# Kernel tuning notes

Hardware: AMD Instinct MI355X
Metric: run time of the kernel (lower is better)

Reference implementation:

```python
import jax, jax.numpy as jnp
import numpy as np

TOKENS_B, TOKENS_S, N_IN, N_OUT = 8, 2048, 4096, 4096
N8, N4 = 2048, 2048  # channels per format


def setup_inputs() -> dict:
    key = jax.random.key(0)
    k = jax.random.split(key, 7)
    x = jax.random.normal(k[0], (TOKENS_B, TOKENS_S, N_IN), dtype=jnp.float32)
    # int8-format group: values in [-128, 127], per-output-channel scale
    q8 = jax.random.randint(k[1], (N8, N_IN), -128, 128, dtype=jnp.int32)
    s8 = jax.random.uniform(k[2], (N8, 1), dtype=jnp.float32) * 0.01 + 1e-4
    # int4-format group: values in [-8, 7], per-output-channel scale
    q4 = jax.random.randint(k[3], (N4, N_IN), -8, 8, dtype=jnp.int32)
    s4 = jax.random.uniform(k[4], (N4, 1), dtype=jnp.float32) * 0.1 + 1e-4
    # inverse permutation restoring original channel order from [fmt8 | fmt4] concat
    inv_perm = jax.random.permutation(k[5], N_OUT).astype(jnp.int32)
    bias = jax.random.normal(k[6], (N_OUT,), dtype=jnp.float32) * 0.01
    return {"x": x, "q8": q8, "s8": s8, "q4": q4, "s4": s4,
            "inv_perm": inv_perm, "bias": bias}


def reference(x, q8, s8, q4, s4, inv_perm, bias):
    # Per-format dequantize: w = q * scale (per-output-channel scale)
    w8 = q8.astype(jnp.float32) * s8  # [N8, N_IN]
    w4 = q4.astype(jnp.float32) * s4  # [N4, N_IN]
    # Grouped GEMMs, one per format
    y8 = jnp.einsum('bsi,oi->bso', x, w8)  # [B, S, N8]
    y4 = jnp.einsum('bsi,oi->bso', x, w4)  # [B, S, N4]
    # Concat along output channels, then restore original channel order
    y = jnp.concatenate([y8, y4], axis=-1)  # [B, S, N_OUT]
    out = y[..., inv_perm] + bias
    return out
```

## Files before the change

### kernel.cpp

```cpp
#include <hip/hip_runtime.h>


#define M_TOK 16384
#define N_O   4096
#define K_IN  4096
#define N8F   2048
#define NT    (K_IN / 128)

typedef __attribute__((ext_vector_type(4))) int i32x4;

__device__ __forceinline__ void gl_lds16(const void* g, void* l) {
  __builtin_amdgcn_global_load_lds(
      (const __attribute__((address_space(1))) unsigned int*)g,
      (__attribute__((address_space(3))) unsigned int*)l, 16, 0, 0);
}

__device__ __forceinline__ int clampq(float f) {
  int q = (int)rintf(f);
  return q > 127 ? 127 : (q < -127 ? -127 : q);
}

__global__ void prep_kernel(const float* __restrict__ x,
                            const int4* __restrict__ q8, const float* __restrict__ s8,
                            const int4* __restrict__ q4, const float* __restrict__ s4,
                            const int* __restrict__ inv,
                            char* __restrict__ Wq, float* __restrict__ scale,
                            float* __restrict__ sx, char* __restrict__ xq) {
  __shared__ float red[4];
  const int t = threadIdx.x;
  if (blockIdx.x < N_O) {
    const int j = blockIdx.x;
    const int c = inv[j];
    const int4* src; float s;
    if (c < N8F) { src = q8 + (size_t)c * (K_IN / 4);         s = s8[c]; }
    else         { src = q4 + (size_t)(c - N8F) * (K_IN / 4); s = s4[c - N8F]; }
    if (t == 0) scale[j] = s;
    unsigned dw[4];
#pragma unroll
    for (int i = 0; i < 4; ++i) {
      int4 v = src[t * 4 + i];
      dw[i] = (v.x & 255) | ((v.y & 255) << 8) | ((v.z & 255) << 16)
            | ((unsigned)(v.w & 255) << 24);
    }
    *(uint4*)(Wq + (size_t)j * K_IN + t * 16) = make_uint4(dw[0], dw[1], dw[2], dw[3]);
  } else {
    const int T = blockIdx.x - N_O;
    const float4* xr = (const float4*)(x + (size_t)T * K_IN);
    float4 v[4];
    float m = 0.f;
#pragma unroll
    for (int i = 0; i < 4; ++i) {
      v[i] = xr[t * 4 + i];
      m = fmaxf(m, fmaxf(fmaxf(fabsf(v[i].x), fabsf(v[i].y)),
                         fmaxf(fabsf(v[i].z), fabsf(v[i].w))));
    }
#pragma unroll
    for (int o = 32; o; o >>= 1) m = fmaxf(m, __shfl_xor(m, o));
    if ((t & 63) == 0) red[t >> 6] = m;
    __syncthreads();
    m = fmaxf(fmaxf(red[0], red[1]), fmaxf(red[2], red[3]));
    const float rq = m > 0.f ? 127.f / m : 0.f;
    if (t == 0) sx[T] = m * (1.f / 127.f);
    unsigned dw[4];
#pragma unroll
    for (int i = 0; i < 4; ++i) {
      int a0 = clampq(v[i].x * rq), a1 = clampq(v[i].y * rq);
      int a2 = clampq(v[i].z * rq), a3 = clampq(v[i].w * rq);
      dw[i] = (a0 & 255) | ((a1 & 255) << 8) | ((a2 & 255) << 16)
            | ((unsigned)(a3 & 255) << 24);
    }
    *(uint4*)(xq + (size_t)T * K_IN + t * 16) = make_uint4(dw[0], dw[1], dw[2], dw[3]);
  }
}

__global__ __launch_bounds__(512, 2)
void gemm_i8(const char* __restrict__ xq, const char* __restrict__ Wq,
             const float* __restrict__ sx, const float* __restrict__ scale,
             const float* __restrict__ bias, float* __restrict__ out) {
  __shared__ __align__(16) char sm[131072];
  const int t = threadIdx.x;
  const int w = t >> 6, l = t & 63;
  const int wr = w >> 2, wc = w & 3;
  const int bm = blockIdx.x >> 4, bn = blockIdx.x & 15;
  const int row0 = bm * 256, col0 = bn * 256;

  const int srow = l >> 3;
  const int schunk = ((l & 7) ^ srow) * 16;
  const char* aG = xq + (size_t)(row0 + w * 16 + srow) * K_IN + schunk;
  const char* bG = Wq + (size_t)(col0 + w * 16 + srow) * K_IN + schunk;
  char* aL0 = sm + w * 2048;
  char* bL0 = sm + 32768 + w * 2048;

  auto stageA = [&](int buf, int kt, int h) {
    const char* g = aG + (size_t)h * (128 * K_IN) + (size_t)kt * 128;
    char* p = aL0 + buf * 65536 + h * 16384;
    gl_lds16(g, p);
    gl_lds16(g + 8 * K_IN, p + 1024);
  };
  auto stageB = [&](int buf, int kt, int h) {
    const char* g = bG + (size_t)h * (128 * K_IN) + (size_t)kt * 128;
    char* p = bL0 + buf * 65536 + h * 16384;
    gl_lds16(g, p);
    gl_lds16(g + 8 * K_IN, p + 1024);
  };

  const int lrow128 = (l & 15) * 128;
  const int cb0 = (((l >> 4) << 4) ^ ((l & 7) << 4));
  const int aWoff = wr * 16384 + lrow128;
  const int bWoff = 32768 + (wc >> 1) * 16384 + (wc & 1) * 8192 + lrow128;

  i32x4 acc[8][4];
#pragma unroll
  for (int m = 0; m < 8; ++m)
#pragma unroll
    for (int n = 0; n < 4; ++n) acc[m][n] = (i32x4){0, 0, 0, 0};

  stageB(0, 0, 0); stageB(0, 0, 1); stageA(0, 0, 0); stageA(0, 0, 1);
  stageB(1, 1, 0); stageB(1, 1, 1); stageA(1, 1, 0);
  asm volatile("s_waitcnt vmcnt(6)" ::: "memory");
  __builtin_amdgcn_s_barrier();

  i32x4 bfr[4][2], afr[2][2], afr2[2][2];

  for (int kt = 0; kt < NT; ++kt) {
    const int cur = kt & 1;
    const char* smA = sm + cur * 65536 + aWoff;
    const char* smB = sm + cur * 65536 + bWoff;

#pragma unroll
    for (int n = 0; n < 4; ++n) {
      bfr[n][0] = *(const i32x4*)(smB + n * 2048 + cb0);
      bfr[n][1] = *(const i32x4*)(smB + n * 2048 + (cb0 ^ 64));
    }
#pragma unroll
    for (int m = 0; m < 2; ++m) {
      afr[m][0] = *(const i32x4*)(smA + m * 2048 + cb0);
      afr[m][1] = *(const i32x4*)(smA + m * 2048 + (cb0 ^ 64));
    }
    if (kt + 1 < NT) stageA(cur ^ 1, kt + 1, 1);
    __builtin_amdgcn_s_barrier();
    asm volatile("s_waitcnt lgkmcnt(0)" ::: "memory");
    __builtin_amdgcn_s_setprio(1);
#pragma unroll
    for (int m = 0; m < 2; ++m)
#pragma unroll
      for (int n = 0; n < 4; ++n)
#pragma unroll
        for (int kk = 0; kk < 2; ++kk)
          acc[m][n] = __builtin_amdgcn_mfma_i32_16x16x64_i8(afr[m][kk], bfr[n][kk],
                                                            acc[m][n], 0, 0, 0);
    __builtin_amdgcn_s_setprio(0);
    __builtin_amdgcn_s_barrier();

#pragma unroll
    for (int m = 0; m < 2; ++m) {
      afr[m][0] = *(const i32x4*)(smA + (2 + m) * 2048 + cb0);
      afr[m][1] = *(const i32x4*)(smA + (2 + m) * 2048 + (cb0 ^ 64));
    }
    if (kt + 2 < NT) stageB(cur, kt + 2, 0);
    __builtin_amdgcn_s_barrier();
    asm volatile("s_waitcnt lgkmcnt(0)" ::: "memory");
    __builtin_amdgcn_s_setprio(1);
#pragma unroll
    for (int m = 0; m < 2; ++m)
#pragma unroll
      for (int n = 0; n < 4; ++n)
#pragma unroll
        for (int kk = 0; kk < 2; ++kk)
          acc[2 + m][n] = __builtin_amdgcn_mfma_i32_16x16x64_i8(afr[m][kk], bfr[n][kk],
                                                                acc[2 + m][n], 0, 0, 0);
    __builtin_amdgcn_s_setprio(0);
    __builtin_amdgcn_s_barrier();

#pragma unroll
    for (int m = 0; m < 2; ++m) {
      afr[m][0]  = *(const i32x4*)(smA + (4 + m) * 2048 + cb0);
      afr[m][1]  = *(const i32x4*)(smA + (4 + m) * 2048 + (cb0 ^ 64));
      afr2[m][0] = *(const i32x4*)(smA + (6 + m) * 2048 + cb0);
      afr2[m][1] = *(const i32x4*)(smA + (6 + m) * 2048 + (cb0 ^ 64));
    }
    if (kt + 2 < NT) stageB(cur, kt + 2, 1);
    __builtin_amdgcn_s_barrier();
    asm volatile("s_waitcnt lgkmcnt(0)" ::: "memory");
    __builtin_amdgcn_s_setprio(1);
#pragma unroll
    for (int m = 0; m < 2; ++m)
#pragma unroll
      for (int n = 0; n < 4; ++n)
#pragma unroll
        for (int kk = 0; kk < 2; ++kk)
          acc[4 + m][n] = __builtin_amdgcn_mfma_i32_16x16x64_i8(afr[m][kk], bfr[n][kk],
                                                                acc[4 + m][n], 0, 0, 0);
    __builtin_amdgcn_s_setprio(0);
    __builtin_amdgcn_s_barrier();

    if (kt + 2 < NT) {
      stageA(cur, kt + 2, 0);
      asm volatile("s_waitcnt vmcnt(6)" ::: "memory");
    } else {
      asm volatile("s_waitcnt vmcnt(0)" ::: "memory");
    }
    __builtin_amdgcn_s_barrier();
    __builtin_amdgcn_s_setprio(1);
#pragma unroll
    for (int m = 0; m < 2; ++m)
#pragma unroll
      for (int n = 0; n < 4; ++n)
#pragma unroll
        for (int kk = 0; kk < 2; ++kk)
          acc[6 + m][n] = __builtin_amdgcn_mfma_i32_16x16x64_i8(afr2[m][kk], bfr[n][kk],
                                                                acc[6 + m][n], 0, 0, 0);
    __builtin_amdgcn_s_setprio(0);
    __builtin_amdgcn_s_barrier();
  }

  const int orow0 = row0 + wr * 128 + ((l >> 4) << 2);
  const int ocol0 = col0 + wc * 64 + (l & 15);
#pragma unroll
  for (int n = 0; n < 4; ++n) {
    const int col = ocol0 + n * 16;
    const float sc = scale[col];
    const float bi = bias[col];
#pragma unroll
    for (int m = 0; m < 8; ++m) {
      const int r = orow0 + m * 16;
      const float4 sxv = *(const float4*)(sx + r);
      out[(size_t)(r + 0) * N_O + col] = (float)acc[m][n][0] * (sxv.x * sc) + bi;
      out[(size_t)(r + 1) * N_O + col] = (float)acc[m][n][1] * (sxv.y * sc) + bi;
      out[(size_t)(r + 2) * N_O + col] = (float)acc[m][n][2] * (sxv.z * sc) + bi;
      out[(size_t)(r + 3) * N_O + col] = (float)acc[m][n][3] * (sxv.w * sc) + bi;
    }
  }
}

extern "C" void kernel_launch(void* const* d_in, const int* in_sizes, int n_in,
                              void* d_out, int out_size, void* d_ws, size_t ws_size,
                              hipStream_t stream) {
  const float* x    = (const float*)d_in[0];
  const int*   q8   = (const int*)d_in[1];
  const float* s8   = (const float*)d_in[2];
  const int*   q4   = (const int*)d_in[3];
  const float* s4   = (const float*)d_in[4];
  const int*   inv  = (const int*)d_in[5];
  const float* bias = (const float*)d_in[6];
  float* out = (float*)d_out;

  char* ws = (char*)d_ws;
  char*  Wq    = ws;
  float* scale = (float*)(ws + (size_t)N_O * K_IN);
  float* sx    = (float*)(ws + (size_t)N_O * K_IN + 65536);
  char*  xq    = ws + (size_t)N_O * K_IN + 65536 + 65536;

  prep_kernel<<<N_O + M_TOK, 256, 0, stream>>>(x, (const int4*)q8, s8,
                                               (const int4*)q4, s4, inv,
                                               Wq, scale, sx, xq);
  gemm_i8<<<(M_TOK / 256) * (N_O / 256), 512, 0, stream>>>(xq, Wq, sx, scale,
                                                           bias, out);
}
```

Measured before the change: 375.3 us.

## Switch int8 GEMM to 32x32x32 MFMA tiles with restructured fragment loads

Replaces the 16x16x64 int8 MFMA tiling with 32x32x32 MFMA instructions on 16-wide accumulators. This cuts the number of MFMA issues and LDS fragment loads per wave tile and raises operand reuse. The K loop is reorganised from four compute phases to two, staging both B halves together and adding sched_barriers. The LDS read offsets and swizzle pattern change, and so does the epilogue's row/column mapping. This carries correctness risk if the swizzle or output layout does not match the 32x32 MFMA lane layout.

```diff
diff --git a/kernel.cpp b/kernel.cpp
--- a/kernel.cpp
+++ b/kernel.cpp
@@ -7,7 +7,8 @@
 #define N8F   2048
 #define NT    (K_IN / 128)
 
-typedef __attribute__((ext_vector_type(4))) int i32x4;
+typedef __attribute__((ext_vector_type(4)))  int i32x4;
+typedef __attribute__((ext_vector_type(16))) int i32x16;
 
 __device__ __forceinline__ void gl_lds16(const void* g, void* l) {
   __builtin_amdgcn_global_load_lds(
@@ -104,93 +105,78 @@
     gl_lds16(g + 8 * K_IN, p + 1024);
   };
 
-  const int lrow128 = (l & 15) * 128;
-  const int cb0 = (((l >> 4) << 4) ^ ((l & 7) << 4));
-  const int aWoff = wr * 16384 + lrow128;
-  const int bWoff = 32768 + (wc >> 1) * 16384 + (wc & 1) * 8192 + lrow128;
-
-  i32x4 acc[8][4];
-#pragma unroll
-  for (int m = 0; m < 8; ++m)
-#pragma unroll
-    for (int n = 0; n < 4; ++n) acc[m][n] = (i32x4){0, 0, 0, 0};
-
-  stageB(0, 0, 0); stageB(0, 0, 1); stageA(0, 0, 0); stageA(0, 0, 1);
+  const int lrow = (l & 31) * 128;
+  const int x0 = (((l >> 5) << 4) ^ ((l & 7) << 4));
+  int off[4];
+#pragma unroll
+  for (int c = 0; c < 4; ++c) off[c] = ((c << 5) ^ x0);
+  const char* rAb = sm + wr * 16384 + lrow;
+  const char* rBb = sm + 32768 + (wc >> 1) * 16384 + (wc & 1) * 8192 + lrow;
+
+  i32x16 acc[4][2];
+#pragma unroll
+  for (int m = 0; m < 4; ++m)
+#pragma unroll
+    for (int n = 0; n < 2; ++n)
+#pragma unroll
+      for (int e = 0; e < 16; ++e) acc[m][n][e] = 0;
+
+  stageA(0, 0, 0); stageA(0, 0, 1); stageB(0, 0, 0); stageB(0, 0, 1);
   stageB(1, 1, 0); stageB(1, 1, 1); stageA(1, 1, 0);
   asm volatile("s_waitcnt vmcnt(6)" ::: "memory");
   __builtin_amdgcn_s_barrier();
 
-  i32x4 bfr[4][2], afr[2][2], afr2[2][2];
+  i32x4 bfr[2][4], afr[2][4];
 
   for (int kt = 0; kt < NT; ++kt) {
     const int cur = kt & 1;
-    const char* smA = sm + cur * 65536 + aWoff;
-    const char* smB = sm + cur * 65536 + bWoff;
-
-#pragma unroll
-    for (int n = 0; n < 4; ++n) {
-      bfr[n][0] = *(const i32x4*)(smB + n * 2048 + cb0);
-      bfr[n][1] = *(const i32x4*)(smB + n * 2048 + (cb0 ^ 64));
-    }
-#pragma unroll
-    for (int m = 0; m < 2; ++m) {
-      afr[m][0] = *(const i32x4*)(smA + m * 2048 + cb0);
-      afr[m][1] = *(const i32x4*)(smA + m * 2048 + (cb0 ^ 64));
-    }
+    const char* rA = rAb + cur * 65536;
+    const char* rB = rBb + cur * 65536;
+
+#pragma unroll
+    for (int n = 0; n < 2; ++n)
+#pragma unroll
+      for (int c = 0; c < 4; ++c)
+        bfr[n][c] = *(const i32x4*)(rB + n * 4096 + off[c]);
+#pragma unroll
+    for (int m = 0; m < 2; ++m)
+#pragma unroll
+      for (int c = 0; c < 4; ++c)
+        afr[m][c] = *(const i32x4*)(rA + m * 4096 + off[c]);
     if (kt + 1 < NT) stageA(cur ^ 1, kt + 1, 1);
     __builtin_amdgcn_s_barrier();
     asm volatile("s_waitcnt lgkmcnt(0)" ::: "memory");
+    __builtin_amdgcn_sched_barrier(0);
     __builtin_amdgcn_s_setprio(1);
 #pragma unroll
-    for (int m = 0; m < 2; ++m)
-#pragma unroll
-      for (int n = 0; n < 4; ++n)
-#pragma unroll
-        for (int kk = 0; kk < 2; ++kk)
-          acc[m][n] = __builtin_amdgcn_mfma_i32_16x16x64_i8(afr[m][kk], bfr[n][kk],
+    for (int c = 0; c < 4; ++c)
+#pragma unroll
+      for (int m = 0; m < 2; ++m)
+#pragma unroll
+        for (int n = 0; n < 2; ++n)
+          acc[m][n] = __builtin_amdgcn_mfma_i32_32x32x32_i8(afr[m][c], bfr[n][c],
                                                             acc[m][n], 0, 0, 0);
     __builtin_amdgcn_s_setprio(0);
     __builtin_amdgcn_s_barrier();
 
 #pragma unroll
-    for (int m = 0; m < 2; ++m) {
-      afr[m][0] = *(const i32x4*)(smA + (2 + m) * 2048 + cb0);
-      afr[m][1] = *(const i32x4*)(smA + (2 + m) * 2048 + (cb0 ^ 64));
-    }
-    if (kt + 2 < NT) stageB(cur, kt + 2, 0);
+    for (int m = 0; m < 2; ++m)
+#pragma unroll
+      for (int c = 0; c < 4; ++c)
+        afr[m][c] = *(const i32x4*)(rA + (2 + m) * 4096 + off[c]);
+    if (kt + 2 < NT) { stageB(cur, kt + 2, 0); stageB(cur, kt + 2, 1); }
     __builtin_amdgcn_s_barrier();
     asm volatile("s_waitcnt lgkmcnt(0)" ::: "memory");
+    __builtin_amdgcn_sched_barrier(0);
     __builtin_amdgcn_s_setprio(1);
 #pragma unroll
-    for (int m = 0; m < 2; ++m)
-#pragma unroll
-      for (int n = 0; n < 4; ++n)
-#pragma unroll
-        for (int kk = 0; kk < 2; ++kk)
-          acc[2 + m][n] = __builtin_amdgcn_mfma_i32_16x16x64_i8(afr[m][kk], bfr[n][kk],
+    for (int c = 0; c < 4; ++c)
+#pragma unroll
+      for (int m = 0; m < 2; ++m)
+#pragma unroll
+        for (int n = 0; n < 2; ++n)
+          acc[2 + m][n] = __builtin_amdgcn_mfma_i32_32x32x32_i8(afr[m][c], bfr[n][c],
                                                                 acc[2 + m][n], 0, 0, 0);
-    __builtin_amdgcn_s_setprio(0);
-    __builtin_amdgcn_s_barrier();
-
-#pragma unroll
-    for (int m = 0; m < 2; ++m) {
-      afr[m][0]  = *(const i32x4*)(smA + (4 + m) * 2048 + cb0);
-      afr[m][1]  = *(const i32x4*)(smA + (4 + m) * 2048 + (cb0 ^ 64));
-      afr2[m][0] = *(const i32x4*)(smA + (6 + m) * 2048 + cb0);
-      afr2[m][1] = *(const i32x4*)(smA + (6 + m) * 2048 + (cb0 ^ 64));
-    }
-    if (kt + 2 < NT) stageB(cur, kt + 2, 1);
-    __builtin_amdgcn_s_barrier();
-    asm volatile("s_waitcnt lgkmcnt(0)" ::: "memory");
-    __builtin_amdgcn_s_setprio(1);
-#pragma unroll
-    for (int m = 0; m < 2; ++m)
-#pragma unroll
-      for (int n = 0; n < 4; ++n)
-#pragma unroll
-        for (int kk = 0; kk < 2; ++kk)
-          acc[4 + m][n] = __builtin_amdgcn_mfma_i32_16x16x64_i8(afr[m][kk], bfr[n][kk],
-                                                                acc[4 + m][n], 0, 0, 0);
     __builtin_amdgcn_s_setprio(0);
     __builtin_amdgcn_s_barrier();
 
@@ -201,34 +187,27 @@
       asm volatile("s_waitcnt vmcnt(0)" ::: "memory");
     }
     __builtin_amdgcn_s_barrier();
-    __builtin_amdgcn_s_setprio(1);
-#pragma unroll
-    for (int m = 0; m < 2; ++m)
-#pragma unroll
-      for (int n = 0; n < 4; ++n)
-#pragma unroll
-        for (int kk = 0; kk < 2; ++kk)
-          acc[6 + m][n] = __builtin_amdgcn_mfma_i32_16x16x64_i8(afr2[m][kk], bfr[n][kk],
-                                                                acc[6 + m][n], 0, 0, 0);
-    __builtin_amdgcn_s_setprio(0);
-    __builtin_amdgcn_s_barrier();
   }
 
-  const int orow0 = row0 + wr * 128 + ((l >> 4) << 2);
-  const int ocol0 = col0 + wc * 64 + (l & 15);
-#pragma unroll
-  for (int n = 0; n < 4; ++n) {
-    const int col = ocol0 + n * 16;
+  const int ocol0 = col0 + wc * 64 + (l & 31);
+  const int orow0 = row0 + wr * 128 + 4 * (l >> 5);
+#pragma unroll
+  for (int n = 0; n < 2; ++n) {
+    const int col = ocol0 + n * 32;
     const float sc = scale[col];
     const float bi = bias[col];
 #pragma unroll
-    for (int m = 0; m < 8; ++m) {
-      const int r = orow0 + m * 16;
-      const float4 sxv = *(const float4*)(sx + r);
-      out[(size_t)(r + 0) * N_O + col] = (float)acc[m][n][0] * (sxv.x * sc) + bi;
-      out[(size_t)(r + 1) * N_O + col] = (float)acc[m][n][1] * (sxv.y * sc) + bi;
-      out[(size_t)(r + 2) * N_O + col] = (float)acc[m][n][2] * (sxv.z * sc) + bi;
-      out[(size_t)(r + 3) * N_O + col] = (float)acc[m][n][3] * (sxv.w * sc) + bi;
+    for (int m = 0; m < 4; ++m) {
+      const int rb = orow0 + m * 32;
+#pragma unroll
+      for (int g = 0; g < 4; ++g) {
+        const int r = rb + 8 * g;
+        const float4 sxv = *(const float4*)(sx + r);
+        out[(size_t)(r + 0) * N_O + col] = (float)acc[m][n][4 * g + 0] * (sxv.x * sc) + bi;
+        out[(size_t)(r + 1) * N_O + col] = (float)acc[m][n][4 * g + 1] * (sxv.y * sc) + bi;
+        out[(size_t)(r + 2) * N_O + col] = (float)acc[m][n][4 * g + 2] * (sxv.z * sc) + bi;
+        out[(size_t)(r + 3) * N_O + col] = (float)acc[m][n][4 * g + 3] * (sxv.w * sc) + bi;
+      }
     }
   }
 }
```

New measurement: 401.3 us. 1.07x slower.
